# Performance work log

Measured on AMD Instinct MI355X. Metric: run time of the kernel, lower is better.

The kernel has to match this reference:

```python
import jax, jax.numpy as jnp
import numpy as np

# Standard SMPL kinematic tree (child -> parent); root's entry unused.
PARENTS = np.array([0, 0, 0, 0, 1, 2, 3, 4, 5, 6, 7, 8, 9, 9, 9, 12, 13, 14, 16, 17, 18, 19, 20, 21], dtype=np.int32)
N_JOINTS = 24


def _rodrigues(r):
    # r: [..., 3] axis-angle -> [..., 3, 3] rotation matrices.
    # Original adds N(0,1e-8) noise to avoid div-by-zero; we use a deterministic eps.
    theta = jnp.linalg.norm(r, axis=-1, keepdims=True) + 1e-8
    rh = r / theta
    cos = jnp.cos(theta)[..., None]
    sin = jnp.sin(theta)[..., None]
    z = jnp.zeros_like(rh[..., 0])
    K = jnp.stack([z, -rh[..., 2], rh[..., 1],
                   rh[..., 2], z, -rh[..., 0],
                   -rh[..., 1], rh[..., 0], z], axis=-1).reshape(r.shape[:-1] + (3, 3))
    outer = rh[..., :, None] * rh[..., None, :]
    eye = jnp.eye(3, dtype=r.dtype)
    return cos * eye + (1.0 - cos) * outer + sin * K


def setup_inputs() -> dict:
    key = jax.random.key(0)
    ks = jax.random.split(key, 7)
    N, V, J, B = 512, 6890, 24, 10
    beta = jax.random.normal(ks[0], (N, B), dtype=jnp.float32)
    pose = jax.random.normal(ks[1], (N, J * 3), dtype=jnp.float32)
    v_template = jax.random.normal(ks[2], (V, 3), dtype=jnp.float32)
    shapedirs = jax.random.normal(ks[3], (V, 3, B), dtype=jnp.float32) * 0.03
    posedirs = jax.random.normal(ks[4], (V, 3, (J - 1) * 9), dtype=jnp.float32) * 0.01
    J_regressor = jax.random.uniform(ks[5], (J, V), dtype=jnp.float32)
    J_regressor = J_regressor / jnp.sum(J_regressor, axis=1, keepdims=True)  # NonNegUnitSum(axis=1)
    weights = jax.random.uniform(ks[6], (V, J), dtype=jnp.float32)
    weights = weights / jnp.sum(weights, axis=1, keepdims=True)  # NonNegUnitSum(axis=1)
    return {"beta": beta, "pose": pose, "v_template": v_template, "shapedirs": shapedirs,
            "posedirs": posedirs, "J_regressor": J_regressor, "weights": weights}


def reference(beta, pose, v_template, shapedirs, posedirs, J_regressor, weights):
    N = beta.shape[0]
    dt = beta.dtype
    # Shape blendshapes: [N,V,3]
    v_shaped = jnp.einsum('nb,vcb->nvc', beta, shapedirs) + v_template
    # Joint locations: [N,J,3]
    J_loc = jnp.einsum('jv,nvc->njc', J_regressor, v_shaped)
    # Per-joint rotations: [N,24,3,3]
    R = _rodrigues(pose.reshape(N, N_JOINTS, 3))
    # Pose blendshapes
    lrotmin = (R[:, 1:] - jnp.eye(3, dtype=dt)).reshape(N, (N_JOINTS - 1) * 9)
    v_posed = v_shaped + jnp.einsum('np,vcp->nvc', lrotmin, posedirs)
    # Kinematic chain of 4x4 transforms
    bottom = jnp.broadcast_to(jnp.array([0.0, 0.0, 0.0, 1.0], dtype=dt), (N, 1, 4))

    def make_T(Rm, t):  # [N,3,3], [N,3] -> [N,4,4]
        return jnp.concatenate([jnp.concatenate([Rm, t[..., None]], axis=-1), bottom], axis=-2)

    G = [make_T(R[:, 0], J_loc[:, 0])]
    for i in range(1, N_JOINTS):
        p = int(PARENTS[i])
        G.append(jnp.matmul(G[p], make_T(R[:, i], J_loc[:, i] - J_loc[:, p])))
    G = jnp.stack(G, axis=1)  # [N,24,4,4]
    # Remove rest-pose joint translation: G[...,:,3] -= G @ [J,0]
    Jh = jnp.concatenate([J_loc, jnp.zeros_like(J_loc[..., :1])], axis=-1)  # [N,24,4]
    RJ = jnp.einsum('njab,njb->nja', G, Jh)
    G = G - jnp.pad(RJ[..., None], ((0, 0), (0, 0), (0, 0), (3, 0)))
    # Linear blend skinning: per-vertex blended transform [N,V,4,4]
    T = jnp.einsum('njab,vj->nvab', G, weights)
    vh = jnp.concatenate([v_posed, jnp.ones_like(v_posed[..., :1])], axis=-1)  # [N,V,4]
    v = jnp.einsum('nvab,nvb->nva', T, vh)
    return v[..., :3]
```

## Files before the change

### kernel.cpp

```cpp
#include <hip/hip_runtime.h>

#define V_CNT 6890
#define N_B 512
#define NP 207
#define KPAD 224
#define RTOT 20670
#define RPAD 20736
#define PREP_BLKS 2268
#define JS1_BLKS 192
#define W_BLKS 27

typedef unsigned short ushort_t;
typedef __attribute__((ext_vector_type(4))) float f32x4;
typedef __attribute__((ext_vector_type(8))) short s16x8;
typedef __attribute__((ext_vector_type(4))) short s16x4;

#define O_PART 0u
#define O_G2   65536u
#define O_A    655360u
#define O_W    917504u
#define O_B    1441792u

__device__ __constant__ int PAR[24] = {0,0,0,0,1,2,3,4,5,6,7,8,9,9,9,12,13,14,16,17,18,19,20,21};
__device__ __constant__ int LVL[36] = {
    1, 2, 3,-1,   4, 5, 6,-1,   7, 8, 9,-1,
   10,11,12,13,  14,-1,-1,-1,  15,16,17,-1,
   18,19,-1,-1,  20,21,-1,-1,  22,23,-1,-1};

__device__ __forceinline__ ushort_t f2bf(float f) {
    union { float f; unsigned u; } x; x.f = f;
    unsigned u = x.u + 0x7fffu + ((x.u >> 16) & 1u);
    return (ushort_t)(u >> 16);
}
__device__ __forceinline__ float bf2f(ushort_t h) {
    union { unsigned u; float f; } x; x.u = ((unsigned)h) << 16;
    return x.f;
}

__global__ __launch_bounds__(256) void k_pre(const float* __restrict__ pdirs,
                                             const float* __restrict__ sdirs,
                                             const float* __restrict__ vtemp,
                                             const float* __restrict__ jreg,
                                             const float* __restrict__ wts,
                                             ushort_t* __restrict__ Bswz,
                                             float* __restrict__ part,
                                             ushort_t* __restrict__ Wp) {
    int b = blockIdx.x;
    int tid = threadIdx.x;
    if (b < PREP_BLKS) {
        int g = b * 256 + tid;
        int rtile = g / 448;
        int rem = g - rtile * 448;
        int kc = rem >> 6;
        int lane = rem & 63;
        int quad = lane >> 4, lm = lane & 15;
        int r = rtile * 16 + lm;
        int k0 = kc * 32 + quad * 8;
        s16x8 pk;
        if (r < RTOT) {
            const float* pr = pdirs + (size_t)r * NP;
            const float* sr = sdirs + (size_t)r * 10;
#pragma unroll
            for (int i = 0; i < 8; i++) {
                int k = k0 + i;
                float v = 0.f;
                if (k < NP) v = pr[k];
                else if (k < 217) v = sr[k - NP];
                pk[i] = (short)f2bf(v);
            }
        } else {
#pragma unroll
            for (int i = 0; i < 8; i++) pk[i] = 0;
        }
        *(s16x8*)(Bswz + (size_t)g * 8) = pk;
    } else if (b < PREP_BLKS + JS1_BLKS) {
        int b2 = b - PREP_BLKS;
        int ch = b2 & 7;
        int j = b2 >> 3;
        int v0 = ch * 862;
        int vend = v0 + 862; if (vend > V_CNT) vend = V_CNT;
        float acc[33];
#pragma unroll
        for (int i = 0; i < 33; i++) acc[i] = 0.f;
        for (int v = v0 + tid; v < vend; v += 256) {
            float r = jreg[j * V_CNT + v];
            const float* sd = sdirs + v * 30;
#pragma unroll
            for (int i = 0; i < 30; i++) acc[i] += r * sd[i];
            acc[30] += r * vtemp[v * 3 + 0];
            acc[31] += r * vtemp[v * 3 + 1];
            acc[32] += r * vtemp[v * 3 + 2];
        }
#pragma unroll
        for (int off = 32; off > 0; off >>= 1) {
#pragma unroll
            for (int i = 0; i < 33; i++) acc[i] += __shfl_down(acc[i], off);
        }
        __shared__ float red[4][33];
        int w = tid >> 6, lane = tid & 63;
        if (lane == 0) {
#pragma unroll
            for (int i = 0; i < 33; i++) red[w][i] = acc[i];
        }
        __syncthreads();
        if (tid < 33) {
            float s = red[0][tid] + red[1][tid] + red[2][tid] + red[3][tid];
            part[b2 * 33 + tid] = s;
        }
    } else {
        int v = (b - PREP_BLKS - JS1_BLKS) * 256 + tid;
        ushort_t o[32];
        if (v < V_CNT) {
            const float* wr = wts + v * 24;
#pragma unroll
            for (int j = 0; j < 24; j++) o[j] = f2bf(wr[j]);
        } else {
#pragma unroll
            for (int j = 0; j < 24; j++) o[j] = 0;
        }
#pragma unroll
        for (int j = 24; j < 32; j++) o[j] = 0;
#pragma unroll
        for (int q = 0; q < 4; q++)
            *(s16x8*)(Wp + (size_t)v * 32 + q * 8) = *(s16x8*)&o[q * 8];
    }
}

__global__ __launch_bounds__(128) void k_chain(const float* __restrict__ beta,
                                               const float* __restrict__ pose,
                                               const float* __restrict__ part,
                                               ushort_t* __restrict__ G2,
                                               ushort_t* __restrict__ Aswz) {
    __shared__ float JSl[720];
    __shared__ float JTl[72];
    __shared__ float Rl[2][24][9];
    __shared__ float Jl[2][24][3];
    __shared__ float Tm[2][24][16];
    __shared__ float G[2][24][16];
    __shared__ float Gp[2][24][12];
    int tid = threadIdx.x;

    for (int t = tid; t < 792; t += 128) {
        int j = t / 33, i = t - j * 33;
        float s = 0.f;
#pragma unroll
        for (int c = 0; c < 8; c++) s += part[(j * 8 + c) * 33 + i];
        if (i < 30) JSl[j * 30 + i] = s;
        else        JTl[j * 3 + (i - 30)] = s;
    }
    __syncthreads();

    int sub = tid >> 6, lane = tid & 63;
    int n = blockIdx.x * 2 + sub;

    if (lane < 24) {
        int t = lane;
        float x = pose[n * 72 + t * 3 + 0];
        float y = pose[n * 72 + t * 3 + 1];
        float z = pose[n * 72 + t * 3 + 2];
        float th = sqrtf(x * x + y * y + z * z) + 1e-8f;
        float inv = 1.f / th;
        float rx = x * inv, ry = y * inv, rz = z * inv;
        float c = cosf(th), s = sinf(th), omc = 1.f - c;
        Rl[sub][t][0] = c + omc * rx * rx;
        Rl[sub][t][1] = omc * rx * ry - s * rz;
        Rl[sub][t][2] = omc * rx * rz + s * ry;
        Rl[sub][t][3] = omc * ry * rx + s * rz;
        Rl[sub][t][4] = c + omc * ry * ry;
        Rl[sub][t][5] = omc * ry * rz - s * rx;
        Rl[sub][t][6] = omc * rz * rx - s * ry;
        Rl[sub][t][7] = omc * rz * ry + s * rx;
        Rl[sub][t][8] = c + omc * rz * rz;
#pragma unroll
        for (int cc = 0; cc < 3; cc++) {
            float a = JTl[t * 3 + cc];
#pragma unroll
            for (int b = 0; b < 10; b++) a += beta[n * 10 + b] * JSl[(t * 3 + cc) * 10 + b];
            Jl[sub][t][cc] = a;
        }
    }
    __syncthreads();
    if (lane < 24) {
        int t = lane;
        int p = PAR[t];
        float tx, ty, tz;
        if (t == 0) { tx = Jl[sub][0][0]; ty = Jl[sub][0][1]; tz = Jl[sub][0][2]; }
        else { tx = Jl[sub][t][0] - Jl[sub][p][0]; ty = Jl[sub][t][1] - Jl[sub][p][1]; tz = Jl[sub][t][2] - Jl[sub][p][2]; }
        Tm[sub][t][0] = Rl[sub][t][0]; Tm[sub][t][1] = Rl[sub][t][1]; Tm[sub][t][2]  = Rl[sub][t][2]; Tm[sub][t][3]  = tx;
        Tm[sub][t][4] = Rl[sub][t][3]; Tm[sub][t][5] = Rl[sub][t][4]; Tm[sub][t][6]  = Rl[sub][t][5]; Tm[sub][t][7]  = ty;
        Tm[sub][t][8] = Rl[sub][t][6]; Tm[sub][t][9] = Rl[sub][t][7]; Tm[sub][t][10] = Rl[sub][t][8]; Tm[sub][t][11] = tz;
        Tm[sub][t][12] = 0.f; Tm[sub][t][13] = 0.f; Tm[sub][t][14] = 0.f; Tm[sub][t][15] = 1.f;
    }
    __syncthreads();
    if (lane < 16) G[sub][0][lane] = Tm[sub][0][lane];
    __syncthreads();
#pragma unroll
    for (int p9 = 0; p9 < 9; p9++) {
        int slot = lane >> 4, el = lane & 15;
        int j = LVL[p9 * 4 + slot];
        if (j >= 0) {
            int par = PAR[j];
            int a = el >> 2, bb = el & 3;
            float s = G[sub][par][a * 4 + 0] * Tm[sub][j][0 * 4 + bb]
                    + G[sub][par][a * 4 + 1] * Tm[sub][j][1 * 4 + bb]
                    + G[sub][par][a * 4 + 2] * Tm[sub][j][2 * 4 + bb]
                    + G[sub][par][a * 4 + 3] * Tm[sub][j][3 * 4 + bb];
            G[sub][j][el] = s;
        }
        __syncthreads();
    }
    if (lane < 24) {
        int t = lane;
        float jx = Jl[sub][t][0], jy = Jl[sub][t][1], jz = Jl[sub][t][2];
#pragma unroll
        for (int a = 0; a < 3; a++) {
            float g0 = G[sub][t][a * 4 + 0], g1 = G[sub][t][a * 4 + 1];
            float g2 = G[sub][t][a * 4 + 2], g3 = G[sub][t][a * 4 + 3];
            Gp[sub][t][a * 4 + 0] = g0;
            Gp[sub][t][a * 4 + 1] = g1;
            Gp[sub][t][a * 4 + 2] = g2;
            Gp[sub][t][a * 4 + 3] = g3 - (g0 * jx + g1 * jy + g2 * jz);
        }
    }
    __syncthreads();
    {
        int quad = lane >> 4, lm = lane & 15;
        s16x8 pk;
#pragma unroll
        for (int jj = 0; jj < 8; jj++) {
            int joint = quad * 8 + jj;
            float val = (joint < 24 && lm < 12) ? Gp[sub][joint][lm] : 0.f;
            pk[jj] = (short)f2bf(val);
        }
        *(s16x8*)(G2 + (size_t)n * 512 + lane * 8) = pk;
    }
    if (lane < 28) {
        int kc = lane >> 2, quad2 = lane & 3;
        s16x8 pk;
#pragma unroll
        for (int j = 0; j < 8; j++) {
            int k = kc * 32 + quad2 * 8 + j;
            float val;
            if (k < NP) {
                int jo = 1 + k / 9;
                int e = k - (jo - 1) * 9;
                float d = (e == 0 || e == 4 || e == 8) ? 1.f : 0.f;
                val = Rl[sub][jo][e] - d;
            } else if (k < 217) {
                val = beta[n * 10 + (k - NP)];
            } else val = 0.f;
            pk[j] = (short)f2bf(val);
        }
        *(s16x8*)(Aswz + (((size_t)(n >> 4) * 7 + kc) * 64 + (quad2 * 16 + (n & 15))) * 8) = pk;
    }
}

__global__ __launch_bounds__(256) void k_fused(const ushort_t* __restrict__ Aswz,
                                               const ushort_t* __restrict__ Bswz,
                                               const ushort_t* __restrict__ Wp,
                                               const ushort_t* __restrict__ G2,
                                               const float* __restrict__ vtemp,
                                               float* __restrict__ out) {
    __shared__ ushort_t vp[4][96][36];
    int tid = threadIdx.x, w = tid >> 6, lane = tid & 63;
    int quad = lane >> 4, lm = lane & 15;
    int rh = w & 1, nh = w >> 1;
    int n_w = blockIdx.y * 64 + nh * 32;
    int vs_w = blockIdx.x * 64 + rh * 32;
    int rtile0 = blockIdx.x * 12 + rh * 6;
    int ntile0 = blockIdx.y * 4 + nh * 2;

    f32x4 acc[2][6];
#pragma unroll
    for (int a = 0; a < 2; a++)
#pragma unroll
        for (int b = 0; b < 6; b++) acc[a][b] = (f32x4)0.f;

    s16x8 af[2][2], bf[2][6];
#pragma unroll
    for (int mt = 0; mt < 2; mt++)
        af[0][mt] = *(const s16x8*)(Aswz + ((size_t)(ntile0 + mt) * 7 + 0) * 512 + lane * 8);
#pragma unroll
    for (int rt = 0; rt < 6; rt++)
        bf[0][rt] = *(const s16x8*)(Bswz + ((size_t)(rtile0 + rt) * 7 + 0) * 512 + lane * 8);
#pragma unroll
    for (int kc = 0; kc < 7; kc++) {
        int cur = kc & 1, nxt = cur ^ 1;
        if (kc < 6) {
#pragma unroll
            for (int mt = 0; mt < 2; mt++)
                af[nxt][mt] = *(const s16x8*)(Aswz + ((size_t)(ntile0 + mt) * 7 + kc + 1) * 512 + lane * 8);
#pragma unroll
            for (int rt = 0; rt < 6; rt++)
                bf[nxt][rt] = *(const s16x8*)(Bswz + ((size_t)(rtile0 + rt) * 7 + kc + 1) * 512 + lane * 8);
        }
#pragma unroll
        for (int mt = 0; mt < 2; mt++)
#pragma unroll
            for (int rt = 0; rt < 6; rt++)
                acc[mt][rt] = __builtin_amdgcn_mfma_f32_16x16x32_bf16(af[cur][mt], bf[cur][rt], acc[mt][rt], 0, 0, 0);
    }

    float vt[6];
#pragma unroll
    for (int rt = 0; rt < 6; rt++) {
        int col = blockIdx.x * 192 + rh * 96 + rt * 16 + lm;
        vt[rt] = (col < RTOT) ? vtemp[col] : 0.f;
    }
#pragma unroll
    for (int mt = 0; mt < 2; mt++) {
#pragma unroll
        for (int rt = 0; rt < 6; rt++) {
            int rl = rt * 16 + lm;
            int nl0 = mt * 16 + quad * 4;
            s16x4 pk;
            pk[0] = (short)f2bf(acc[mt][rt][0] + vt[rt]);
            pk[1] = (short)f2bf(acc[mt][rt][1] + vt[rt]);
            pk[2] = (short)f2bf(acc[mt][rt][2] + vt[rt]);
            pk[3] = (short)f2bf(acc[mt][rt][3] + vt[rt]);
            *(s16x4*)&vp[w][rl][nl0] = pk;
        }
    }

    s16x8 wf[2];
#pragma unroll
    for (int mt = 0; mt < 2; mt++)
        wf[mt] = *(const s16x8*)(Wp + (size_t)(vs_w + mt * 16 + lm) * 32 + quad * 8);

    s16x8 ga = *(const s16x8*)(G2 + (size_t)n_w * 512 + lane * 8);
    s16x8 gb = *(const s16x8*)(G2 + (size_t)(n_w + 1) * 512 + lane * 8);
#pragma unroll 1
    for (int t = 0; t < 16; t++) {
        int na = n_w + 2 * t;
        s16x8 gan, gbn;
        if (t < 15) {
            gan = *(const s16x8*)(G2 + (size_t)(na + 2) * 512 + lane * 8);
            gbn = *(const s16x8*)(G2 + (size_t)(na + 3) * 512 + lane * 8);
        }
        f32x4 ta[2], tb[2];
#pragma unroll
        for (int mt = 0; mt < 2; mt++) {
            ta[mt] = __builtin_amdgcn_mfma_f32_16x16x32_bf16(ga, wf[mt], (f32x4)0.f, 0, 0, 0);
            tb[mt] = __builtin_amdgcn_mfma_f32_16x16x32_bf16(gb, wf[mt], (f32x4)0.f, 0, 0, 0);
        }
        if (quad < 3) {
#pragma unroll
            for (int mt = 0; mt < 2; mt++) {
                int v = vs_w + mt * 16 + lm;
                if (v < V_CNT) {
                    int vloc = mt * 16 + lm;
                    unsigned pw0 = *(const unsigned*)&vp[w][vloc * 3 + 0][2 * t];
                    unsigned pw1 = *(const unsigned*)&vp[w][vloc * 3 + 1][2 * t];
                    unsigned pw2 = *(const unsigned*)&vp[w][vloc * 3 + 2][2 * t];
                    float p0a = bf2f((ushort_t)(pw0 & 0xffffu)), p0b = bf2f((ushort_t)(pw0 >> 16));
                    float p1a = bf2f((ushort_t)(pw1 & 0xffffu)), p1b = bf2f((ushort_t)(pw1 >> 16));
                    float p2a = bf2f((ushort_t)(pw2 & 0xffffu)), p2b = bf2f((ushort_t)(pw2 >> 16));
                    float oa = ta[mt][3] + ta[mt][0] * p0a + ta[mt][1] * p1a + ta[mt][2] * p2a;
                    float ob = tb[mt][3] + tb[mt][0] * p0b + tb[mt][1] * p1b + tb[mt][2] * p2b;
                    out[((size_t)na * V_CNT + v) * 3 + quad] = oa;
                    out[((size_t)(na + 1) * V_CNT + v) * 3 + quad] = ob;
                }
            }
        }
        ga = gan; gb = gbn;
    }
}

extern "C" void kernel_launch(void* const* d_in, const int* in_sizes, int n_in,
                              void* d_out, int out_size, void* d_ws, size_t ws_size,
                              hipStream_t stream) {
    const float* beta  = (const float*)d_in[0];
    const float* pose  = (const float*)d_in[1];
    const float* vtemp = (const float*)d_in[2];
    const float* sdirs = (const float*)d_in[3];
    const float* pdirs = (const float*)d_in[4];
    const float* jreg  = (const float*)d_in[5];
    const float* wts   = (const float*)d_in[6];
    char* ws = (char*)d_ws;
    float*    ws_part = (float*)(ws + O_PART);
    ushort_t* ws_G2   = (ushort_t*)(ws + O_G2);
    ushort_t* ws_A    = (ushort_t*)(ws + O_A);
    ushort_t* ws_W    = (ushort_t*)(ws + O_W);
    ushort_t* ws_B    = (ushort_t*)(ws + O_B);
    float* out = (float*)d_out;

    k_pre<<<dim3(PREP_BLKS + JS1_BLKS + W_BLKS), dim3(256), 0, stream>>>(
        pdirs, sdirs, vtemp, jreg, wts, ws_B, ws_part, ws_W);
    k_chain<<<dim3(N_B / 2), dim3(128), 0, stream>>>(beta, pose, ws_part, ws_G2, ws_A);
    k_fused<<<dim3(108, N_B / 64), dim3(256), 0, stream>>>(ws_A, ws_B, ws_W, ws_G2, vtemp, out);
}
```

Measured before the change: 138.4 us.

## Merge three kernels into one cooperative persistent kernel with grid syncs

Replaces the prep, chain and fused kernels with a single cooperative launch of 864 blocks. Two grid-wide barriers separate the stages, and prep work is spread across blocks so it overlaps with the joint regression and chain stages. The chain stage now handles 4 samples per 256-thread block. The fused GEMM drops its register double-buffering of A/B/G2 loads in favour of simple per-iteration loads, which lowers register pressure for the 4-blocks-per-CU occupancy needed for residency. A fallback path launches the three kernels separately if the cooperative launch fails.

```diff
diff --git a/kernel.cpp b/kernel.cpp
--- a/kernel.cpp
+++ b/kernel.cpp
@@ -1,14 +1,17 @@
 #include <hip/hip_runtime.h>
+#include <hip/hip_cooperative_groups.h>
+namespace cg = cooperative_groups;
 
 #define V_CNT 6890
 #define N_B 512
 #define NP 207
-#define KPAD 224
 #define RTOT 20670
-#define RPAD 20736
-#define PREP_BLKS 2268
-#define JS1_BLKS 192
-#define W_BLKS 27
+#define PREP_UNITS 2268
+#define ALL_UNITS 2295
+#define JS1_UNITS 192
+#define CHAIN_UNITS 128
+#define FUSE_X 108
+#define FUSE_BLKS 864
 
 typedef unsigned short ushort_t;
 typedef __attribute__((ext_vector_type(4))) float f32x4;
@@ -37,18 +40,14 @@
     return x.f;
 }
 
-__global__ __launch_bounds__(256) void k_pre(const float* __restrict__ pdirs,
-                                             const float* __restrict__ sdirs,
-                                             const float* __restrict__ vtemp,
-                                             const float* __restrict__ jreg,
-                                             const float* __restrict__ wts,
-                                             ushort_t* __restrict__ Bswz,
-                                             float* __restrict__ part,
-                                             ushort_t* __restrict__ Wp) {
-    int b = blockIdx.x;
-    int tid = threadIdx.x;
-    if (b < PREP_BLKS) {
-        int g = b * 256 + tid;
+__device__ __forceinline__ void dev_prep(int p, int tid,
+                                         const float* __restrict__ pdirs,
+                                         const float* __restrict__ sdirs,
+                                         const float* __restrict__ wts,
+                                         ushort_t* __restrict__ Bswz,
+                                         ushort_t* __restrict__ Wp) {
+    if (p < PREP_UNITS) {
+        int g = p * 256 + tid;
         int rtile = g / 448;
         int rem = g - rtile * 448;
         int kc = rem >> 6;
@@ -73,42 +72,8 @@
             for (int i = 0; i < 8; i++) pk[i] = 0;
         }
         *(s16x8*)(Bswz + (size_t)g * 8) = pk;
-    } else if (b < PREP_BLKS + JS1_BLKS) {
-        int b2 = b - PREP_BLKS;
-        int ch = b2 & 7;
-        int j = b2 >> 3;
-        int v0 = ch * 862;
-        int vend = v0 + 862; if (vend > V_CNT) vend = V_CNT;
-        float acc[33];
-#pragma unroll
-        for (int i = 0; i < 33; i++) acc[i] = 0.f;
-        for (int v = v0 + tid; v < vend; v += 256) {
-            float r = jreg[j * V_CNT + v];
-            const float* sd = sdirs + v * 30;
-#pragma unroll
-            for (int i = 0; i < 30; i++) acc[i] += r * sd[i];
-            acc[30] += r * vtemp[v * 3 + 0];
-            acc[31] += r * vtemp[v * 3 + 1];
-            acc[32] += r * vtemp[v * 3 + 2];
-        }
-#pragma unroll
-        for (int off = 32; off > 0; off >>= 1) {
-#pragma unroll
-            for (int i = 0; i < 33; i++) acc[i] += __shfl_down(acc[i], off);
-        }
-        __shared__ float red[4][33];
-        int w = tid >> 6, lane = tid & 63;
-        if (lane == 0) {
-#pragma unroll
-            for (int i = 0; i < 33; i++) red[w][i] = acc[i];
-        }
-        __syncthreads();
-        if (tid < 33) {
-            float s = red[0][tid] + red[1][tid] + red[2][tid] + red[3][tid];
-            part[b2 * 33 + tid] = s;
-        }
     } else {
-        int v = (b - PREP_BLKS - JS1_BLKS) * 256 + tid;
+        int v = (p - PREP_UNITS) * 256 + tid;
         ushort_t o[32];
         if (v < V_CNT) {
             const float* wr = wts + v * 24;
@@ -126,21 +91,64 @@
     }
 }
 
-__global__ __launch_bounds__(128) void k_chain(const float* __restrict__ beta,
-                                               const float* __restrict__ pose,
-                                               const float* __restrict__ part,
-                                               ushort_t* __restrict__ G2,
-                                               ushort_t* __restrict__ Aswz) {
-    __shared__ float JSl[720];
-    __shared__ float JTl[72];
-    __shared__ float Rl[2][24][9];
-    __shared__ float Jl[2][24][3];
-    __shared__ float Tm[2][24][16];
-    __shared__ float G[2][24][16];
-    __shared__ float Gp[2][24][12];
-    int tid = threadIdx.x;
-
-    for (int t = tid; t < 792; t += 128) {
+__device__ __forceinline__ void dev_js1(int b2, int tid,
+                                        const float* __restrict__ jreg,
+                                        const float* __restrict__ sdirs,
+                                        const float* __restrict__ vtemp,
+                                        float* __restrict__ part,
+                                        char* smemc) {
+    int ch = b2 & 7;
+    int j = b2 >> 3;
+    int v0 = ch * 862;
+    int vend = v0 + 862; if (vend > V_CNT) vend = V_CNT;
+    float acc[33];
+#pragma unroll
+    for (int i = 0; i < 33; i++) acc[i] = 0.f;
+    for (int v = v0 + tid; v < vend; v += 256) {
+        float r = jreg[j * V_CNT + v];
+        const float* sd = sdirs + v * 30;
+#pragma unroll
+        for (int i = 0; i < 30; i++) acc[i] += r * sd[i];
+        acc[30] += r * vtemp[v * 3 + 0];
+        acc[31] += r * vtemp[v * 3 + 1];
+        acc[32] += r * vtemp[v * 3 + 2];
+    }
+#pragma unroll
+    for (int off = 32; off > 0; off >>= 1) {
+#pragma unroll
+        for (int i = 0; i < 33; i++) acc[i] += __shfl_down(acc[i], off);
+    }
+    float (*red)[33] = (float (*)[33])smemc;
+    int w = tid >> 6, lane = tid & 63;
+    if (lane == 0) {
+#pragma unroll
+        for (int i = 0; i < 33; i++) red[w][i] = acc[i];
+    }
+    __syncthreads();
+    if (tid < 33) {
+        float s = red[0][tid] + red[1][tid] + red[2][tid] + red[3][tid];
+        part[b2 * 33 + tid] = s;
+    }
+    __syncthreads();
+}
+
+__device__ __forceinline__ void dev_chain4(int u, int tid,
+                                           const float* __restrict__ beta,
+                                           const float* __restrict__ pose,
+                                           const float* __restrict__ part,
+                                           ushort_t* __restrict__ G2,
+                                           ushort_t* __restrict__ Aswz,
+                                           char* smemc) {
+    float* smem_f = (float*)smemc;
+    float* JSl = smem_f;
+    float* JTl = smem_f + 720;
+    float (*Rl)[24][9]  = (float (*)[24][9])(smem_f + 792);
+    float (*Jl)[24][3]  = (float (*)[24][3])(smem_f + 1656);
+    float (*Tm)[24][16] = (float (*)[24][16])(smem_f + 1944);
+    float (*G )[24][16] = (float (*)[24][16])(smem_f + 3480);
+    float (*Gp)[24][12] = (float (*)[24][12])(smem_f + 5016);
+
+    for (int t = tid; t < 792; t += 256) {
         int j = t / 33, i = t - j * 33;
         float s = 0.f;
 #pragma unroll
@@ -151,7 +159,7 @@
     __syncthreads();
 
     int sub = tid >> 6, lane = tid & 63;
-    int n = blockIdx.x * 2 + sub;
+    int n = u * 4 + sub;
 
     if (lane < 24) {
         int t = lane;
@@ -253,22 +261,25 @@
         }
         *(s16x8*)(Aswz + (((size_t)(n >> 4) * 7 + kc) * 64 + (quad2 * 16 + (n & 15))) * 8) = pk;
     }
-}
-
-__global__ __launch_bounds__(256) void k_fused(const ushort_t* __restrict__ Aswz,
-                                               const ushort_t* __restrict__ Bswz,
-                                               const ushort_t* __restrict__ Wp,
-                                               const ushort_t* __restrict__ G2,
-                                               const float* __restrict__ vtemp,
-                                               float* __restrict__ out) {
-    __shared__ ushort_t vp[4][96][36];
-    int tid = threadIdx.x, w = tid >> 6, lane = tid & 63;
+    __syncthreads();
+}
+
+__device__ __forceinline__ void dev_fused(int bx, int by, int tid,
+                                          const ushort_t* __restrict__ Aswz,
+                                          const ushort_t* __restrict__ Bswz,
+                                          const ushort_t* __restrict__ Wp,
+                                          const ushort_t* __restrict__ G2,
+                                          const float* __restrict__ vtemp,
+                                          float* __restrict__ out,
+                                          char* smemc) {
+    ushort_t (*vp)[96][36] = (ushort_t (*)[96][36])smemc;
+    int w = tid >> 6, lane = tid & 63;
     int quad = lane >> 4, lm = lane & 15;
     int rh = w & 1, nh = w >> 1;
-    int n_w = blockIdx.y * 64 + nh * 32;
-    int vs_w = blockIdx.x * 64 + rh * 32;
-    int rtile0 = blockIdx.x * 12 + rh * 6;
-    int ntile0 = blockIdx.y * 4 + nh * 2;
+    int n_w = by * 64 + nh * 32;
+    int vs_w = bx * 64 + rh * 32;
+    int rtile0 = bx * 12 + rh * 6;
+    int ntile0 = by * 4 + nh * 2;
 
     f32x4 acc[2][6];
 #pragma unroll
@@ -276,35 +287,26 @@
 #pragma unroll
         for (int b = 0; b < 6; b++) acc[a][b] = (f32x4)0.f;
 
-    s16x8 af[2][2], bf[2][6];
-#pragma unroll
-    for (int mt = 0; mt < 2; mt++)
-        af[0][mt] = *(const s16x8*)(Aswz + ((size_t)(ntile0 + mt) * 7 + 0) * 512 + lane * 8);
-#pragma unroll
-    for (int rt = 0; rt < 6; rt++)
-        bf[0][rt] = *(const s16x8*)(Bswz + ((size_t)(rtile0 + rt) * 7 + 0) * 512 + lane * 8);
-#pragma unroll
+#pragma unroll 1
     for (int kc = 0; kc < 7; kc++) {
-        int cur = kc & 1, nxt = cur ^ 1;
-        if (kc < 6) {
-#pragma unroll
-            for (int mt = 0; mt < 2; mt++)
-                af[nxt][mt] = *(const s16x8*)(Aswz + ((size_t)(ntile0 + mt) * 7 + kc + 1) * 512 + lane * 8);
+        s16x8 af[2], bf[6];
+#pragma unroll
+        for (int mt = 0; mt < 2; mt++)
+            af[mt] = *(const s16x8*)(Aswz + ((size_t)(ntile0 + mt) * 7 + kc) * 512 + lane * 8);
+#pragma unroll
+        for (int rt = 0; rt < 6; rt++)
+            bf[rt] = *(const s16x8*)(Bswz + ((size_t)(rtile0 + rt) * 7 + kc) * 512 + lane * 8);
+#pragma unroll
+        for (int mt = 0; mt < 2; mt++)
 #pragma unroll
             for (int rt = 0; rt < 6; rt++)
-                bf[nxt][rt] = *(const s16x8*)(Bswz + ((size_t)(rtile0 + rt) * 7 + kc + 1) * 512 + lane * 8);
-        }
-#pragma unroll
-        for (int mt = 0; mt < 2; mt++)
-#pragma unroll
-            for (int rt = 0; rt < 6; rt++)
-                acc[mt][rt] = __builtin_amdgcn_mfma_f32_16x16x32_bf16(af[cur][mt], bf[cur][rt], acc[mt][rt], 0, 0, 0);
+                acc[mt][rt] = __builtin_amdgcn_mfma_f32_16x16x32_bf16(af[mt], bf[rt], acc[mt][rt], 0, 0, 0);
     }
 
     float vt[6];
 #pragma unroll
     for (int rt = 0; rt < 6; rt++) {
-        int col = blockIdx.x * 192 + rh * 96 + rt * 16 + lm;
+        int col = bx * 192 + rh * 96 + rt * 16 + lm;
         vt[rt] = (col < RTOT) ? vtemp[col] : 0.f;
     }
 #pragma unroll
@@ -327,16 +329,11 @@
     for (int mt = 0; mt < 2; mt++)
         wf[mt] = *(const s16x8*)(Wp + (size_t)(vs_w + mt * 16 + lm) * 32 + quad * 8);
 
-    s16x8 ga = *(const s16x8*)(G2 + (size_t)n_w * 512 + lane * 8);
-    s16x8 gb = *(const s16x8*)(G2 + (size_t)(n_w + 1) * 512 + lane * 8);
 #pragma unroll 1
     for (int t = 0; t < 16; t++) {
         int na = n_w + 2 * t;
-        s16x8 gan, gbn;
-        if (t < 15) {
-            gan = *(const s16x8*)(G2 + (size_t)(na + 2) * 512 + lane * 8);
-            gbn = *(const s16x8*)(G2 + (size_t)(na + 3) * 512 + lane * 8);
-        }
+        s16x8 ga = *(const s16x8*)(G2 + (size_t)na * 512 + lane * 8);
+        s16x8 gb = *(const s16x8*)(G2 + (size_t)(na + 1) * 512 + lane * 8);
         f32x4 ta[2], tb[2];
 #pragma unroll
         for (int mt = 0; mt < 2; mt++) {
@@ -362,8 +359,83 @@
                 }
             }
         }
-        ga = gan; gb = gbn;
-    }
+    }
+}
+
+__global__ __launch_bounds__(256, 4) void k_all(const float* __restrict__ beta,
+                                                const float* __restrict__ pose,
+                                                const float* __restrict__ vtemp,
+                                                const float* __restrict__ sdirs,
+                                                const float* __restrict__ pdirs,
+                                                const float* __restrict__ jreg,
+                                                const float* __restrict__ wts,
+                                                float* __restrict__ part,
+                                                ushort_t* __restrict__ G2,
+                                                ushort_t* __restrict__ Aswz,
+                                                ushort_t* __restrict__ Wp,
+                                                ushort_t* __restrict__ Bswz,
+                                                float* __restrict__ out) {
+    __shared__ __align__(16) char smem[27648];
+    cg::grid_group grid = cg::this_grid();
+    int bid = blockIdx.x, tid = threadIdx.x;
+
+    if (bid < JS1_UNITS) {
+        dev_js1(bid, tid, jreg, sdirs, vtemp, part, smem);
+    } else {
+        int u0 = bid - JS1_UNITS;
+        dev_prep(u0, tid, pdirs, sdirs, wts, Bswz, Wp);
+        dev_prep(u0 + 672, tid, pdirs, sdirs, wts, Bswz, Wp);
+    }
+    grid.sync();
+
+    if (bid < CHAIN_UNITS) {
+        dev_chain4(bid, tid, beta, pose, part, G2, Aswz, smem);
+    } else {
+        int u = 1344 + (bid - CHAIN_UNITS);
+        if (u < ALL_UNITS) dev_prep(u, tid, pdirs, sdirs, wts, Bswz, Wp);
+        u += 736;
+        if (u < ALL_UNITS) dev_prep(u, tid, pdirs, sdirs, wts, Bswz, Wp);
+    }
+    grid.sync();
+
+    {
+        int uu = (bid & 7) * FUSE_X + (bid >> 3);
+        int bx = uu >> 3, by = uu & 7;
+        dev_fused(bx, by, tid, Aswz, Bswz, Wp, G2, vtemp, out, smem);
+    }
+}
+
+__global__ __launch_bounds__(256) void k_pre2(const float* __restrict__ pdirs,
+                                              const float* __restrict__ sdirs,
+                                              const float* __restrict__ vtemp,
+                                              const float* __restrict__ jreg,
+                                              const float* __restrict__ wts,
+                                              ushort_t* __restrict__ Bswz,
+                                              float* __restrict__ part,
+                                              ushort_t* __restrict__ Wp) {
+    __shared__ __align__(16) char smem[544];
+    int b = blockIdx.x;
+    if (b < JS1_UNITS) dev_js1(b, threadIdx.x, jreg, sdirs, vtemp, part, smem);
+    else dev_prep(b - JS1_UNITS, threadIdx.x, pdirs, sdirs, wts, Bswz, Wp);
+}
+
+__global__ __launch_bounds__(256) void k_chain2(const float* __restrict__ beta,
+                                                const float* __restrict__ pose,
+                                                const float* __restrict__ part,
+                                                ushort_t* __restrict__ G2,
+                                                ushort_t* __restrict__ Aswz) {
+    __shared__ __align__(16) char smem[24672];
+    dev_chain4(blockIdx.x, threadIdx.x, beta, pose, part, G2, Aswz, smem);
+}
+
+__global__ __launch_bounds__(256) void k_fused2(const ushort_t* __restrict__ Aswz,
+                                                const ushort_t* __restrict__ Bswz,
+                                                const ushort_t* __restrict__ Wp,
+                                                const ushort_t* __restrict__ G2,
+                                                const float* __restrict__ vtemp,
+                                                float* __restrict__ out) {
+    __shared__ __align__(16) char smem[27648];
+    dev_fused(blockIdx.x, blockIdx.y, threadIdx.x, Aswz, Bswz, Wp, G2, vtemp, out, smem);
 }
 
 extern "C" void kernel_launch(void* const* d_in, const int* in_sizes, int n_in,
@@ -384,8 +456,17 @@
     ushort_t* ws_B    = (ushort_t*)(ws + O_B);
     float* out = (float*)d_out;
 
-    k_pre<<<dim3(PREP_BLKS + JS1_BLKS + W_BLKS), dim3(256), 0, stream>>>(
-        pdirs, sdirs, vtemp, jreg, wts, ws_B, ws_part, ws_W);
-    k_chain<<<dim3(N_B / 2), dim3(128), 0, stream>>>(beta, pose, ws_part, ws_G2, ws_A);
-    k_fused<<<dim3(108, N_B / 64), dim3(256), 0, stream>>>(ws_A, ws_B, ws_W, ws_G2, vtemp, out);
-}
+    void* args[13] = {(void*)&beta, (void*)&pose, (void*)&vtemp, (void*)&sdirs,
+                      (void*)&pdirs, (void*)&jreg, (void*)&wts, (void*)&ws_part,
+                      (void*)&ws_G2, (void*)&ws_A, (void*)&ws_W, (void*)&ws_B,
+                      (void*)&out};
+    hipError_t err = hipLaunchCooperativeKernel(reinterpret_cast<void*>(k_all),
+                                                dim3(FUSE_BLKS), dim3(256),
+                                                args, 0, stream);
+    if (err != hipSuccess) {
+        k_pre2<<<dim3(JS1_UNITS + ALL_UNITS), dim3(256), 0, stream>>>(
+            pdirs, sdirs, vtemp, jreg, wts, ws_B, ws_part, ws_W);
+        k_chain2<<<dim3(CHAIN_UNITS), dim3(256), 0, stream>>>(beta, pose, ws_part, ws_G2, ws_A);
+        k_fused2<<<dim3(FUSE_X, N_B / 64), dim3(256), 0, stream>>>(ws_A, ws_B, ws_W, ws_G2, vtemp, out);
+    }
+}
```

Result: slower. 355.3 us (+156.6%).
